# Kernel optimization log

Hardware: AMD Instinct MI355X
Metric: run time of the kernel (lower is better)

Reference implementation:

```python
import jax, jax.numpy as jnp
import numpy as np

N_MELS = 20
NUM_FRAMES = 32
FRAME_LEN = 512
SR = NUM_FRAMES * FRAME_LEN  # 16384
EPS = np.finfo(np.float64).eps  # matches np.finfo(float).eps in original


def _mel_filters(n_fft, sr, n_mels, fmin, fmax):
    """Replicates librosa.filters.mel(..., htk=False, norm=None) in pure numpy."""
    f_sp = 200.0 / 3.0
    min_log_hz = 1000.0
    min_log_mel = min_log_hz / f_sp
    logstep = np.log(6.4) / 27.0

    def hz_to_mel(f):
        f = np.asarray(f, dtype=np.float64)
        return np.where(f >= min_log_hz,
                        min_log_mel + np.log(np.maximum(f, 1e-10) / min_log_hz) / logstep,
                        f / f_sp)

    def mel_to_hz(m):
        m = np.asarray(m, dtype=np.float64)
        return np.where(m >= min_log_mel,
                        min_log_hz * np.exp(logstep * (m - min_log_mel)),
                        f_sp * m)

    fftfreqs = np.linspace(0.0, sr / 2.0, 1 + n_fft // 2)
    mels = np.linspace(hz_to_mel(fmin), hz_to_mel(fmax), n_mels + 2)
    mel_f = mel_to_hz(mels)
    fdiff = np.diff(mel_f)
    ramps = mel_f[:, None] - fftfreqs[None, :]
    lower = -ramps[:-2] / fdiff[:-1, None]
    upper = ramps[2:] / fdiff[1:, None]
    weights = np.maximum(0.0, np.minimum(lower, upper))  # norm=None -> no scaling
    return weights.astype(np.float32)  # (n_mels, 1+n_fft//2)


def setup_inputs() -> dict:
    key = jax.random.key(0)
    inputs = jax.random.normal(key, (4096, NUM_FRAMES, FRAME_LEN), dtype=jnp.float32)
    filter_banks = jnp.asarray(_mel_filters(FRAME_LEN, SR, N_MELS, 0.0, SR / 2.0 + 1.0))
    hw = jnp.asarray(np.hamming(FRAME_LEN).astype(np.float32))
    return {"inputs": inputs, "filter_banks": filter_banks, "hw": hw}


def reference(inputs, filter_banks, hw):
    # Hamming window + forward-normalized rFFT; original squares only the REAL part.
    fft_real = jnp.fft.rfft(inputs * hw, norm="forward").real  # (B, 32, 257)
    mag = fft_real * fft_real
    mels = jnp.einsum("mf,btf->btm", filter_banks, mag)  # (B, 32, 20)
    mels = jnp.where(mels == 0, jnp.float32(EPS), mels)
    log_mels = jnp.log2(mels)
    return jnp.floor(log_mels)[..., None]  # (B, 32, 20, 1)
```

## Files before the change

### kernel.cpp

```cpp
#include <hip/hip_runtime.h>
#include <math.h>


#define MARGIN_L2 1.0e-3f
#define IDX(e) ((e) + ((e) >> 3))
#define WCSTRIDE 20

__device__ __forceinline__ float4 f4add(float4 a, float4 b) {
    return make_float4(a.x + b.x, a.y + b.y, a.z + b.z, a.w + b.w);
}
__device__ __forceinline__ float4 f4sub(float4 a, float4 b) {
    return make_float4(a.x - b.x, a.y - b.y, a.z - b.z, a.w - b.w);
}
__device__ __forceinline__ float4 cmulc4(float2 w, float4 z) {
    return make_float4(w.x * z.x + w.y * z.y, w.x * z.y - w.y * z.x,
                       w.x * z.z + w.y * z.w, w.x * z.w - w.y * z.z);
}
__device__ __forceinline__ double2 d2add(double2 a, double2 b) {
    return make_double2(a.x + b.x, a.y + b.y);
}
__device__ __forceinline__ double2 d2sub(double2 a, double2 b) {
    return make_double2(a.x - b.x, a.y - b.y);
}
__device__ __forceinline__ double2 cmulcd(double2 w, double2 z) {
    return make_double2(w.x * z.x + w.y * z.y, w.x * z.y - w.y * z.x);
}

__device__ __forceinline__ void bfly4(int s, int l, float2 w1, float2 w2,
                                      float4 x1, float4 y1, float4 x2, float4 y2,
                                      float4* dst) {
    const int j = l >> s;
    const int r = l & ((1 << s) - 1);
    const float4 u1 = f4add(x1, y1);
    const float4 v1 = cmulc4(w1, f4sub(x1, y1));
    const float4 u2 = f4add(x2, y2);
    const float4 m  = cmulc4(w1, f4sub(x2, y2));
    const float4 v2 = make_float4(m.y, -m.x, m.w, -m.z);
    const float4 o0 = f4add(u1, u2);
    const float4 o1 = cmulc4(w2, f4sub(u1, u2));
    const float4 o2 = f4add(v1, v2);
    const float4 o3 = cmulc4(w2, f4sub(v1, v2));
    const int eb = (j << (s + 2)) + r;
    dst[IDX(eb)]            = o0;
    dst[IDX(eb + (1 << s))] = o2;
    dst[IDX(eb + (2 << s))] = o1;
    dst[IDX(eb + (3 << s))] = o3;
}

__device__ __forceinline__ void bfly4d(int s, int l, double2 w1, double2 w2,
                                       double2 x1, double2 y1, double2 x2,
                                       double2 y2, double2* dst) {
    const int j = l >> s;
    const int r = l & ((1 << s) - 1);
    const double2 u1 = d2add(x1, y1);
    const double2 v1 = cmulcd(w1, d2sub(x1, y1));
    const double2 u2 = d2add(x2, y2);
    const double2 m  = cmulcd(w1, d2sub(x2, y2));
    const double2 v2 = make_double2(m.y, -m.x);
    const double2 o0 = d2add(u1, u2);
    const double2 o1 = cmulcd(w2, d2sub(u1, u2));
    const double2 o2 = d2add(v1, v2);
    const double2 o3 = cmulcd(w2, d2sub(v1, v2));
    const int eb = (j << (s + 2)) + r;
    dst[IDX(eb)]            = o0;
    dst[IDX(eb + (1 << s))] = o2;
    dst[IDX(eb + (2 << s))] = o1;
    dst[IDX(eb + (3 << s))] = o3;
}

__device__ __forceinline__ void load_stage0(
    const float* __restrict__ x, int f0, int f1, int l,
    float2 h0, float2 h1, float2 h2, float2 h3,
    float2 w1, float2 w2, float4* W)
{
    const float2* xa = (const float2*)(x + (size_t)f0 * 512);
    const float2* xb = (const float2*)(x + (size_t)f1 * 512);
    const float2 a0 = xa[l],       a1 = xa[l + 64];
    const float2 a2 = xa[l + 128], a3 = xa[l + 192];
    const float2 b0 = xb[l],       b1 = xb[l + 64];
    const float2 b2 = xb[l + 128], b3 = xb[l + 192];
    const float4 x1 = make_float4(a0.x * h0.x, a0.y * h0.y,
                                  b0.x * h0.x, b0.y * h0.y);
    const float4 x2 = make_float4(a1.x * h1.x, a1.y * h1.y,
                                  b1.x * h1.x, b1.y * h1.y);
    const float4 y1 = make_float4(a2.x * h2.x, a2.y * h2.y,
                                  b2.x * h2.x, b2.y * h2.y);
    const float4 y2 = make_float4(a3.x * h3.x, a3.y * h3.y,
                                  b3.x * h3.x, b3.y * h3.y);
    bfly4(0, l, w1, w2, x1, y1, x2, y2, W);
}

__global__ void prep_full(const float* __restrict__ fb,
                          double* __restrict__ tw64,
                          float4* __restrict__ twp,
                          double4* __restrict__ twq,
                          float4* __restrict__ wc,
                          int*    __restrict__ meta,
                          unsigned* count) {
    __shared__ float2 s_tw[256];
    __shared__ double sc[256], ss[256];
    __shared__ int slo[20], shi[20], sg0[20], sng[20];
    const int t = threadIdx.x;
    double s, c;
    sincospi((double)t * (1.0 / 256.0), &s, &c);
    tw64[t]       = c;
    tw64[256 + t] = s;
    sc[t] = c; ss[t] = s;
    s_tw[t] = make_float2((float)c, (float)s);
    if (t < 20) { slo[t] = 257; shi[t] = 0; }
    __syncthreads();

    if (t < 240) {
        const int m = t / 12, part = t % 12;
        const int k0 = part * 22;
        int k1 = k0 + 22; if (k1 > 257) k1 = 257;
        int lo = 257, hi = 0;
        for (int k = k0; k < k1; k++)
            if (fb[m * 257 + k] > 0.0f) { if (k < lo) lo = k; hi = k + 1; }
        if (hi > lo) { atomicMin(&slo[m], lo); atomicMax(&shi[m], hi); }
    }
    __syncthreads();

    if (t < 20) {
        int lo = slo[t], hi = shi[t];
        if (hi <= lo) { lo = 0; hi = 1; }
        int g0 = lo >> 2;
        int ng = ((hi + 3) >> 2) - g0;
        if (ng > WCSTRIDE) ng = WCSTRIDE;
        sg0[t] = g0; sng[t] = ng;
        meta[t] = g0 | (ng << 16);
    }
    if (t < 64) {
        const float2 a0 = s_tw[2 * t],        b0 = s_tw[4 * t];
        twp[t]        = make_float4(a0.x, a0.y, b0.x, b0.y);
        const float2 a2 = s_tw[8 * (t >> 2)], b2 = s_tw[16 * (t >> 2)];
        twp[64 + t]   = make_float4(a2.x, a2.y, b2.x, b2.y);
        const float2 a4 = s_tw[32 * (t >> 4)], b4 = s_tw[64 * (t >> 4)];
        twp[128 + t]  = make_float4(a4.x, a4.y, b4.x, b4.y);
        const float2 u0 = s_tw[t],            u1 = s_tw[t + 64];
        twp[192 + t]  = make_float4(u0.x, u0.y, u1.x, u1.y);
        twq[t]       = make_double4(sc[2*t], ss[2*t], sc[4*t], ss[4*t]);
        twq[64 + t]  = make_double4(sc[8*(t>>2)],  ss[8*(t>>2)],
                                    sc[16*(t>>2)], ss[16*(t>>2)]);
        twq[128 + t] = make_double4(sc[32*(t>>4)], ss[32*(t>>4)],
                                    sc[64*(t>>4)], ss[64*(t>>4)]);
        twq[192 + t] = make_double4(sc[t], ss[t], sc[t+64], ss[t+64]);
    }
    __syncthreads();

    for (int i = t; i < 20 * WCSTRIDE; i += 256) {
        const int m = i / WCSTRIDE, j = i % WCSTRIDE;
        float4 v = make_float4(0.0f, 0.0f, 0.0f, 0.0f);
        if (j < sng[m]) {
            const int b = (sg0[m] + j) * 4;
            const float* row = fb + m * 257;
            v.x = (b + 0 < 257) ? row[b + 0] : 0.0f;
            v.y = (b + 1 < 257) ? row[b + 1] : 0.0f;
            v.z = (b + 2 < 257) ? row[b + 2] : 0.0f;
            v.w = (b + 3 < 257) ? row[b + 3] : 0.0f;
        }
        wc[i] = v;
    }
    if (count && t == 0) *count = 0;
}

__global__ void prep_tw64(double* __restrict__ tw64) {
    const int t = threadIdx.x;
    double s, c;
    sincospi((double)t * (1.0 / 256.0), &s, &c);
    tw64[t]       = c;
    tw64[256 + t] = s;
}

__global__ __launch_bounds__(256, 4) void phase1(
    const float* __restrict__ x,
    const float* __restrict__ hw,
    const float4* __restrict__ twp,
    const float4* __restrict__ wc,
    const int*    __restrict__ meta,
    float* __restrict__ out,
    unsigned* __restrict__ count,
    unsigned* __restrict__ worklist)
{
    __shared__ __align__(16) float4 buf[8][288];

    const int t = threadIdx.x;
    const int w = t >> 6;
    const int l = t & 63;
    const int base = (blockIdx.x * 4 + w) * 4;
    const int fg0 = base, fg1 = base + 1, fg2 = base + 2, fg3 = base + 3;

    const float4 tp0 = twp[l];
    const float4 tp2 = twp[64 + l];
    const float4 tp4 = twp[128 + l];
    const float4 tpU = twp[192 + l];
    const float2 w0s = make_float2(tp0.x, tp0.y), w0d = make_float2(tp0.z, tp0.w);
    const float2 w2s = make_float2(tp2.x, tp2.y), w2d = make_float2(tp2.z, tp2.w);
    const float2 w4s = make_float2(tp4.x, tp4.y), w4d = make_float2(tp4.z, tp4.w);

    float4* const WA = &buf[2 * w][0];
    float4* const WB = &buf[2 * w + 1][0];

    const float2* hp = (const float2*)hw;
    const float2 h0 = hp[l],       h1 = hp[l + 64];
    const float2 h2 = hp[l + 128], h3 = hp[l + 192];

    load_stage0(x, fg0, fg1, l, h0, h1, h2, h3, w0s, w0d, WA);
    load_stage0(x, fg2, fg3, l, h0, h1, h2, h3, w0s, w0d, WB);
    __builtin_amdgcn_wave_barrier();

    {
        const float4 ax1 = WA[IDX(l)],      ay1 = WA[IDX(l + 128)];
        const float4 ax2 = WA[IDX(l + 64)], ay2 = WA[IDX(l + 192)];
        const float4 bx1 = WB[IDX(l)],      by1 = WB[IDX(l + 128)];
        const float4 bx2 = WB[IDX(l + 64)], by2 = WB[IDX(l + 192)];
        bfly4(2, l, w2s, w2d, ax1, ay1, ax2, ay2, WA);
        bfly4(2, l, w2s, w2d, bx1, by1, bx2, by2, WB);
        __builtin_amdgcn_wave_barrier();
    }
    {
        const float4 ax1 = WA[IDX(l)],      ay1 = WA[IDX(l + 128)];
        const float4 ax2 = WA[IDX(l + 64)], ay2 = WA[IDX(l + 192)];
        const float4 bx1 = WB[IDX(l)],      by1 = WB[IDX(l + 128)];
        const float4 bx2 = WB[IDX(l + 64)], by2 = WB[IDX(l + 192)];
        bfly4(4, l, w4s, w4d, ax1, ay1, ax2, ay2, WA);
        bfly4(4, l, w4s, w4d, bx1, by1, bx2, by2, WB);
        __builtin_amdgcn_wave_barrier();
    }
    {
        const float4 ax1 = WA[IDX(l)],      ay1 = WA[IDX(l + 128)];
        const float4 ax2 = WA[IDX(l + 64)], ay2 = WA[IDX(l + 192)];
        const float4 bx1 = WB[IDX(l)],      by1 = WB[IDX(l + 128)];
        const float4 bx2 = WB[IDX(l + 64)], by2 = WB[IDX(l + 192)];
        {
            const float4 u1 = f4add(ax1, ay1);
            const float4 v1 = f4sub(ax1, ay1);
            const float4 u2 = f4add(ax2, ay2);
            const float4 m  = f4sub(ax2, ay2);
            const float4 v2 = make_float4(m.y, -m.x, m.w, -m.z);
            WA[IDX(l)]       = f4add(u1, u2);
            WA[IDX(l + 64)]  = f4add(v1, v2);
            WA[IDX(l + 128)] = f4sub(u1, u2);
            WA[IDX(l + 192)] = f4sub(v1, v2);
        }
        {
            const float4 u1 = f4add(bx1, by1);
            const float4 v1 = f4sub(bx1, by1);
            const float4 u2 = f4add(bx2, by2);
            const float4 m  = f4sub(bx2, by2);
            const float4 v2 = make_float4(m.y, -m.x, m.w, -m.z);
            WB[IDX(l)]       = f4add(u1, u2);
            WB[IDX(l + 64)]  = f4add(v1, v2);
            WB[IDX(l + 128)] = f4sub(u1, u2);
            WB[IDX(l + 192)] = f4sub(v1, v2);
        }
    }
    __builtin_amdgcn_wave_barrier();

    float2* const pwrA = (float2*)WA;
    float2* const pwrB = (float2*)WB;
    {
        const float4 zk0A = WA[IDX(l)];
        const float4 zc0A = WA[IDX((256 - l) & 255)];
        const float4 zk1A = WA[IDX(l + 64)];
        const float4 zc1A = WA[IDX(192 - l)];
        const float4 zmA  = WA[IDX(128)];
        const float4 zk0B = WB[IDX(l)];
        const float4 zc0B = WB[IDX((256 - l) & 255)];
        const float4 zk1B = WB[IDX(l + 64)];
        const float4 zc1B = WB[IDX(192 - l)];
        const float4 zmB  = WB[IDX(128)];
        const float2 u0 = make_float2(tpU.x, tpU.y);
        const float2 u1 = make_float2(tpU.z, tpU.w);
        __builtin_amdgcn_wave_barrier();

#define UNTANGLE_PAIR(zk, zc, wk, p, kk, kc)                                 \
        {                                                                    \
            const float Sr0 = zk.x + zc.x, Si0 = zk.y + zc.y;                \
            const float Dr0 = zk.x - zc.x;                                   \
            const float Sr1 = zk.z + zc.z, Si1 = zk.w + zc.w;                \
            const float Dr1 = zk.z - zc.z;                                   \
            const float E0 = 0.5f * Sr0;                                     \
            const float T0 = 0.5f * (wk.x * Si0 - wk.y * Dr0);               \
            const float E1 = 0.5f * Sr1;                                     \
            const float T1 = 0.5f * (wk.x * Si1 - wk.y * Dr1);               \
            const float a0 = (E0 + T0) * (1.0f / 512.0f);                    \
            const float a1 = (E1 + T1) * (1.0f / 512.0f);                    \
            const float b0 = (E0 - T0) * (1.0f / 512.0f);                    \
            const float b1 = (E1 - T1) * (1.0f / 512.0f);                    \
            p[kk] = make_float2(a0 * a0, a1 * a1);                           \
            p[kc] = make_float2(b0 * b0, b1 * b1);                           \
        }
        UNTANGLE_PAIR(zk0A, zc0A, u0, pwrA, l, 256 - l)
        UNTANGLE_PAIR(zk1A, zc1A, u1, pwrA, l + 64, 192 - l)
        UNTANGLE_PAIR(zk0B, zc0B, u0, pwrB, l, 256 - l)
        UNTANGLE_PAIR(zk1B, zc1B, u1, pwrB, l + 64, 192 - l)
#undef UNTANGLE_PAIR
        if (l == 0) {
            const float vA0 = zmA.x * (1.0f / 512.0f);
            const float vA1 = zmA.z * (1.0f / 512.0f);
            pwrA[128] = make_float2(vA0 * vA0, vA1 * vA1);
            const float vB0 = zmB.x * (1.0f / 512.0f);
            const float vB1 = zmB.z * (1.0f / 512.0f);
            pwrB[128] = make_float2(vB0 * vB0, vB1 * vB1);
        }
        if (l >= 57) {
            pwrA[257 + (l - 57)] = make_float2(0.0f, 0.0f);
            pwrB[257 + (l - 57)] = make_float2(0.0f, 0.0f);
        }
    }
    __builtin_amdgcn_wave_barrier();

    float aA = 0.0f, aB = 0.0f, aC = 0.0f, aD = 0.0f;
    if (l < 60) {
        const int mel = l % 20;
        const int sub = l / 20;
        const int mw  = meta[mel];
        const int g0m = mw & 0xffff;
        const int ngm = mw >> 16;
        const float4* wrow = wc + mel * WCSTRIDE;
        const float4* pwA4 = (const float4*)pwrA + 2 * g0m;
        const float4* pwB4 = (const float4*)pwrB + 2 * g0m;
        for (int j = sub; j < ngm; j += 3) {
            const float4 w4  = wrow[j];
            const float4 qa0 = pwA4[2 * j];
            const float4 qa1 = pwA4[2 * j + 1];
            const float4 qb0 = pwB4[2 * j];
            const float4 qb1 = pwB4[2 * j + 1];
            aA = fmaf(w4.w, qa1.z, fmaf(w4.z, qa1.x,
                 fmaf(w4.y, qa0.z, fmaf(w4.x, qa0.x, aA))));
            aB = fmaf(w4.w, qa1.w, fmaf(w4.z, qa1.y,
                 fmaf(w4.y, qa0.w, fmaf(w4.x, qa0.y, aB))));
            aC = fmaf(w4.w, qb1.z, fmaf(w4.z, qb1.x,
                 fmaf(w4.y, qb0.z, fmaf(w4.x, qb0.x, aC))));
            aD = fmaf(w4.w, qb1.w, fmaf(w4.z, qb1.y,
                 fmaf(w4.y, qb0.w, fmaf(w4.x, qb0.y, aD))));
        }
    }
    const float pA1 = __shfl(aA, l + 20), pA2 = __shfl(aA, l + 40);
    const float pB1 = __shfl(aB, l + 20), pB2 = __shfl(aB, l + 40);
    const float pC1 = __shfl(aC, l + 20), pC2 = __shfl(aC, l + 40);
    const float pD1 = __shfl(aD, l + 20), pD2 = __shfl(aD, l + 40);

    int fl0 = 0, fl1 = 0, fl2 = 0, fl3 = 0;
    if (l < 20) {
#define FINISH(acc, p1, p2, fg, flag)                                        \
        {                                                                    \
            const float v = acc + p1 + p2;                                   \
            float fl;                                                        \
            if (v < 1e-30f) { fl = -52.0f; flag = 1; }                       \
            else {                                                           \
                const float l2 = log2f(v);                                   \
                fl = floorf(l2);                                             \
                flag = (l2 - fl < MARGIN_L2) | ((fl + 1.0f - l2) < MARGIN_L2);\
            }                                                                \
            out[(size_t)fg * 20 + l] = fl;                                   \
        }
        FINISH(aA, pA1, pA2, fg0, fl0)
        FINISH(aB, pB1, pB2, fg1, fl1)
        FINISH(aC, pC1, pC2, fg2, fl2)
        FINISH(aD, pD1, pD2, fg3, fl3)
#undef FINISH
    }
    const unsigned long long b0 = __ballot(fl0);
    const unsigned long long b1 = __ballot(fl1);
    const unsigned long long b2 = __ballot(fl2);
    const unsigned long long b3 = __ballot(fl3);
    if (l == 0) {
        const unsigned nf = (b0 != 0ULL) + (b1 != 0ULL)
                          + (b2 != 0ULL) + (b3 != 0ULL);
        if (nf) {
            unsigned idx = atomicAdd(count, nf);
            if (b0 != 0ULL) worklist[idx++] = (unsigned)fg0;
            if (b1 != 0ULL) worklist[idx++] = (unsigned)fg1;
            if (b2 != 0ULL) worklist[idx++] = (unsigned)fg2;
            if (b3 != 0ULL) worklist[idx]   = (unsigned)fg3;
        }
    }
}

__global__ __launch_bounds__(256, 4) void phase2_wl(
    const float* __restrict__ x,
    const float* __restrict__ hw,
    const double4* __restrict__ twq,
    const float4* __restrict__ wc,
    const int*    __restrict__ meta,
    const unsigned* __restrict__ count,
    const unsigned* __restrict__ worklist,
    float* __restrict__ out)
{
    __shared__ __align__(16) double2 dbuf[4][288];

    const int t = threadIdx.x;
    const int w = t >> 6;
    const int l = t & 63;
    double2* const W = &dbuf[w][0];
    double* const pwr = (double*)W;

    const unsigned n = *count;
    const unsigned stride = gridDim.x * 4;
    for (unsigned i = blockIdx.x * 4 + (unsigned)w; i < n; i += stride) {
        const int f = (int)worklist[i];

        {
            const double4 tq = twq[l];
            const float2* xa = (const float2*)(x + (size_t)f * 512);
            const float2* hp = (const float2*)hw;
            const float2 a0 = xa[l],       a1 = xa[l + 64];
            const float2 a2 = xa[l + 128], a3 = xa[l + 192];
            const float2 h0 = hp[l],       h1 = hp[l + 64];
            const float2 h2 = hp[l + 128], h3 = hp[l + 192];
            const double2 x1 = make_double2((double)a0.x * (double)h0.x,
                                            (double)a0.y * (double)h0.y);
            const double2 x2 = make_double2((double)a1.x * (double)h1.x,
                                            (double)a1.y * (double)h1.y);
            const double2 y1 = make_double2((double)a2.x * (double)h2.x,
                                            (double)a2.y * (double)h2.y);
            const double2 y2 = make_double2((double)a3.x * (double)h3.x,
                                            (double)a3.y * (double)h3.y);
            bfly4d(0, l, make_double2(tq.x, tq.y), make_double2(tq.z, tq.w),
                   x1, y1, x2, y2, W);
        }
        __builtin_amdgcn_wave_barrier();
        {
            const double4 tq = twq[64 + l];
            const double2 x1 = W[IDX(l)],      y1 = W[IDX(l + 128)];
            const double2 x2 = W[IDX(l + 64)], y2 = W[IDX(l + 192)];
            bfly4d(2, l, make_double2(tq.x, tq.y), make_double2(tq.z, tq.w),
                   x1, y1, x2, y2, W);
        }
        __builtin_amdgcn_wave_barrier();
        {
            const double4 tq = twq[128 + l];
            const double2 x1 = W[IDX(l)],      y1 = W[IDX(l + 128)];
            const double2 x2 = W[IDX(l + 64)], y2 = W[IDX(l + 192)];
            bfly4d(4, l, make_double2(tq.x, tq.y), make_double2(tq.z, tq.w),
                   x1, y1, x2, y2, W);
        }
        __builtin_amdgcn_wave_barrier();
        {
            const double2 x1 = W[IDX(l)],      y1 = W[IDX(l + 128)];
            const double2 x2 = W[IDX(l + 64)], y2 = W[IDX(l + 192)];
            const double2 u1 = d2add(x1, y1);
            const double2 v1 = d2sub(x1, y1);
            const double2 u2 = d2add(x2, y2);
            const double2 m  = d2sub(x2, y2);
            const double2 v2 = make_double2(m.y, -m.x);
            W[IDX(l)]       = d2add(u1, u2);
            W[IDX(l + 64)]  = d2add(v1, v2);
            W[IDX(l + 128)] = d2sub(u1, u2);
            W[IDX(l + 192)] = d2sub(v1, v2);
        }
        __builtin_amdgcn_wave_barrier();
        {
            const double4 tq = twq[192 + l];
            const double2 zk0 = W[IDX(l)];
            const double2 zc0 = W[IDX((256 - l) & 255)];
            const double2 zk1 = W[IDX(l + 64)];
            const double2 zc1 = W[IDX(192 - l)];
            const double2 zm  = W[IDX(128)];
            __builtin_amdgcn_wave_barrier();
            {
                const double Sr = zk0.x + zc0.x, Si = zk0.y + zc0.y;
                const double Dr = zk0.x - zc0.x;
                const double E = 0.5 * Sr, T = 0.5 * (tq.x * Si - tq.y * Dr);
                const double a = (E + T) * (1.0 / 512.0);
                const double b = (E - T) * (1.0 / 512.0);
                pwr[l]       = a * a;
                pwr[256 - l] = b * b;
            }
            {
                const double Sr = zk1.x + zc1.x, Si = zk1.y + zc1.y;
                const double Dr = zk1.x - zc1.x;
                const double E = 0.5 * Sr, T = 0.5 * (tq.z * Si - tq.w * Dr);
                const double a = (E + T) * (1.0 / 512.0);
                const double b = (E - T) * (1.0 / 512.0);
                pwr[l + 64]  = a * a;
                pwr[192 - l] = b * b;
            }
            if (l == 0) {
                const double v = zm.x * (1.0 / 512.0);
                pwr[128] = v * v;
            }
            if (l < 3) pwr[257 + l] = 0.0;
        }
        __builtin_amdgcn_wave_barrier();

        double acc = 0.0;
        if (l < 60) {
            const int mel = l % 20;
            const int sub = l / 20;
            const int mw  = meta[mel];
            const int g0m = mw & 0xffff;
            const int ngm = mw >> 16;
            const float4* wrow = wc + mel * WCSTRIDE;
            const double2* pw2 = (const double2*)pwr + 2 * g0m;
            for (int j = sub; j < ngm; j += 3) {
                const float4 w4 = wrow[j];
                const double2 q0 = pw2[2 * j];
                const double2 q1 = pw2[2 * j + 1];
                acc = fma((double)w4.x, q0.x, acc);
                acc = fma((double)w4.y, q0.y, acc);
                acc = fma((double)w4.z, q1.x, acc);
                acc = fma((double)w4.w, q1.y, acc);
            }
        }
        const double p1 = __shfl(acc, l + 20);
        const double p2 = __shfl(acc, l + 40);
        if (l < 20) {
            double v = acc + p1 + p2;
            if (v == 0.0) v = 2.220446049250313e-16;
            out[(size_t)f * 20 + l] = (float)floor(log2(v));
        }
        __builtin_amdgcn_wave_barrier();
    }
}

__global__ __launch_bounds__(256) void f64_all(
    const float*  __restrict__ x,
    const float*  __restrict__ fb,
    const float*  __restrict__ hw,
    const double* __restrict__ tw,
    float* __restrict__ out)
{
    __shared__ double Are[256], Aim[256], Bre[256], Bim[256];
    __shared__ double ltc[256], lts[256];
    __shared__ double pwr[257];

    const int t = threadIdx.x;
    const int f = blockIdx.x;

    ltc[t] = tw[t];
    lts[t] = tw[256 + t];
    {
        const float2 xv = ((const float2*)x)[(size_t)f * 256 + t];
        const float2 hv = ((const float2*)hw)[t];
        Are[t] = (double)xv.x * (double)hv.x;
        Aim[t] = (double)xv.y * (double)hv.y;
    }
    __syncthreads();

    double* sre = Are; double* sim = Aim;
    double* dre = Bre; double* dim = Bim;
    const int p = t & 127;
    const int which = t >> 7;
#pragma unroll
    for (int s = 0; s < 8; s++) {
        const int j = p >> s;
        const double ar = sre[p],       ai = sim[p];
        const double br = sre[p + 128], bi = sim[p + 128];
        double orr, oi;
        int dpos;
        if (which) {
            const int idx = j << (s + 1);
            const double wr = ltc[idx];
            const double wi = -lts[idx];
            const double ur = ar - br, ui = ai - bi;
            orr = wr * ur - wi * ui;
            oi  = wr * ui + wi * ur;
            dpos = p + ((j + 1) << s);
        } else {
            orr = ar + br;
            oi  = ai + bi;
            dpos = p + (j << s);
        }
        dre[dpos] = orr;
        dim[dpos] = oi;
        __syncthreads();
        double* tmp;
        tmp = sre; sre = dre; dre = tmp;
        tmp = sim; sim = dim; dim = tmp;
    }

    {
        const double a = sre[t], b = sim[t];
        const int t2 = (256 - t) & 255;
        const double c = sre[t2], d = sim[t2];
        const double rex = 0.5 * (a + c)
                         + 0.5 * (ltc[t] * (b + d) - lts[t] * (a - c));
        const double v = rex * (1.0 / 512.0);
        pwr[t] = v * v;
        if (t == 0) {
            const double vn = (a - b) * (1.0 / 512.0);
            pwr[256] = vn * vn;
        }
    }
    __syncthreads();

    if (t < 160) {
        const int mel = t >> 3;
        const int sub = t & 7;
        const float* wrow = fb + mel * 257;
        double acc = 0.0;
        for (int k = sub; k < 257; k += 8)
            acc = fma((double)wrow[k], pwr[k], acc);
        acc += __shfl_down(acc, 4, 8);
        acc += __shfl_down(acc, 2, 8);
        acc += __shfl_down(acc, 1, 8);
        if (sub == 0) {
            double v = acc;
            if (v == 0.0) v = 2.220446049250313e-16;
            out[(size_t)f * 20 + mel] = (float)floor(log2(v));
        }
    }
}

extern "C" void kernel_launch(void* const* d_in, const int* in_sizes, int n_in,
                              void* d_out, int out_size, void* d_ws, size_t ws_size,
                              hipStream_t stream) {
    const float* x  = (const float*)d_in[0];
    const float* fb = (const float*)d_in[1];
    const float* hw = (const float*)d_in[2];
    float* out = (float*)d_out;

    const int frames = in_sizes[0] / 512;

    char* ws = (char*)d_ws;
    double*  tw64 = (double*)ws;
    float4*  twp  = (float4*)(ws + 4096);
    float4*  wc   = (float4*)(ws + 8192);
    int*     meta = (int*)(ws + 14592);
    double4* twq  = (double4*)(ws + 16384);

    const size_t T1 = 32832 + 4 * (size_t)frames;

    if (ws_size >= T1 && (frames % 16) == 0) {
        unsigned* count    = (unsigned*)(ws + 32768);
        unsigned* worklist = (unsigned*)(ws + 32832);
        prep_full<<<1, 256, 0, stream>>>(fb, tw64, twp, twq, wc, meta, count);
        phase1<<<frames / 16, 256, 0, stream>>>(x, hw, twp, wc, meta, out,
                                                count, worklist);
        phase2_wl<<<2048, 256, 0, stream>>>(x, hw, twq, wc, meta,
                                            count, worklist, out);
    } else {
        prep_tw64<<<1, 256, 0, stream>>>(tw64);
        f64_all<<<frames, 256, 0, stream>>>(x, fb, hw, tw64, out);
    }
}
```

Measured before the change: 378.5 us.

## Fuse f64 repair of borderline frames into phase1, drop worklist kernel

Frames whose float32 log2 result falls near an integer boundary are no longer pushed to a global worklist for a separate double-precision kernel. Each wave now recomputes its flagged frames in double precision inline, through a noinline device function that reuses the wave's shared buffer. This removes the third kernel launch, the atomic worklist append and the count reset. The cost is that flagged frames are serialized inside phase1 waves, and the extra code may raise register or occupancy pressure in phase1.

```diff
diff --git a/kernel.cpp b/kernel.cpp
--- a/kernel.cpp
+++ b/kernel.cpp
@@ -90,21 +90,138 @@
     bfly4(0, l, w1, w2, x1, y1, x2, y2, W);
 }
 
+__device__ __attribute__((noinline)) void repair_f64(
+    const float* __restrict__ x, const float* __restrict__ hw,
+    const double4* __restrict__ twq, const float4* __restrict__ wc,
+    const int* __restrict__ meta, float* __restrict__ out,
+    int f, int l, double2* W)
+{
+    double* const pwr = (double*)W;
+
+    {
+        const double4 tq = twq[l];
+        const float2* xa = (const float2*)(x + (size_t)f * 512);
+        const float2* hp = (const float2*)hw;
+        const float2 a0 = xa[l],       a1 = xa[l + 64];
+        const float2 a2 = xa[l + 128], a3 = xa[l + 192];
+        const float2 h0 = hp[l],       h1 = hp[l + 64];
+        const float2 h2 = hp[l + 128], h3 = hp[l + 192];
+        const double2 x1 = make_double2((double)a0.x * (double)h0.x,
+                                        (double)a0.y * (double)h0.y);
+        const double2 x2 = make_double2((double)a1.x * (double)h1.x,
+                                        (double)a1.y * (double)h1.y);
+        const double2 y1 = make_double2((double)a2.x * (double)h2.x,
+                                        (double)a2.y * (double)h2.y);
+        const double2 y2 = make_double2((double)a3.x * (double)h3.x,
+                                        (double)a3.y * (double)h3.y);
+        bfly4d(0, l, make_double2(tq.x, tq.y), make_double2(tq.z, tq.w),
+               x1, y1, x2, y2, W);
+    }
+    __builtin_amdgcn_wave_barrier();
+    {
+        const double4 tq = twq[64 + l];
+        const double2 x1 = W[IDX(l)],      y1 = W[IDX(l + 128)];
+        const double2 x2 = W[IDX(l + 64)], y2 = W[IDX(l + 192)];
+        bfly4d(2, l, make_double2(tq.x, tq.y), make_double2(tq.z, tq.w),
+               x1, y1, x2, y2, W);
+    }
+    __builtin_amdgcn_wave_barrier();
+    {
+        const double4 tq = twq[128 + l];
+        const double2 x1 = W[IDX(l)],      y1 = W[IDX(l + 128)];
+        const double2 x2 = W[IDX(l + 64)], y2 = W[IDX(l + 192)];
+        bfly4d(4, l, make_double2(tq.x, tq.y), make_double2(tq.z, tq.w),
+               x1, y1, x2, y2, W);
+    }
+    __builtin_amdgcn_wave_barrier();
+    {
+        const double2 x1 = W[IDX(l)],      y1 = W[IDX(l + 128)];
+        const double2 x2 = W[IDX(l + 64)], y2 = W[IDX(l + 192)];
+        const double2 u1 = d2add(x1, y1);
+        const double2 v1 = d2sub(x1, y1);
+        const double2 u2 = d2add(x2, y2);
+        const double2 m  = d2sub(x2, y2);
+        const double2 v2 = make_double2(m.y, -m.x);
+        W[IDX(l)]       = d2add(u1, u2);
+        W[IDX(l + 64)]  = d2add(v1, v2);
+        W[IDX(l + 128)] = d2sub(u1, u2);
+        W[IDX(l + 192)] = d2sub(v1, v2);
+    }
+    __builtin_amdgcn_wave_barrier();
+    {
+        const double4 tq = twq[192 + l];
+        const double2 zk0 = W[IDX(l)];
+        const double2 zc0 = W[IDX((256 - l) & 255)];
+        const double2 zk1 = W[IDX(l + 64)];
+        const double2 zc1 = W[IDX(192 - l)];
+        const double2 zm  = W[IDX(128)];
+        __builtin_amdgcn_wave_barrier();
+        {
+            const double Sr = zk0.x + zc0.x, Si = zk0.y + zc0.y;
+            const double Dr = zk0.x - zc0.x;
+            const double E = 0.5 * Sr, T = 0.5 * (tq.x * Si - tq.y * Dr);
+            const double a = (E + T) * (1.0 / 512.0);
+            const double b = (E - T) * (1.0 / 512.0);
+            pwr[l]       = a * a;
+            pwr[256 - l] = b * b;
+        }
+        {
+            const double Sr = zk1.x + zc1.x, Si = zk1.y + zc1.y;
+            const double Dr = zk1.x - zc1.x;
+            const double E = 0.5 * Sr, T = 0.5 * (tq.z * Si - tq.w * Dr);
+            const double a = (E + T) * (1.0 / 512.0);
+            const double b = (E - T) * (1.0 / 512.0);
+            pwr[l + 64]  = a * a;
+            pwr[192 - l] = b * b;
+        }
+        if (l == 0) {
+            const double v = zm.x * (1.0 / 512.0);
+            pwr[128] = v * v;
+        }
+        if (l < 3) pwr[257 + l] = 0.0;
+    }
+    __builtin_amdgcn_wave_barrier();
+
+    double acc = 0.0;
+    if (l < 60) {
+        const int mel = l % 20;
+        const int sub = l / 20;
+        const int mw  = meta[mel];
+        const int g0m = mw & 0xffff;
+        const int ngm = mw >> 16;
+        const float4* wrow = wc + mel * WCSTRIDE;
+        const double2* pw2 = (const double2*)pwr + 2 * g0m;
+        for (int j = sub; j < ngm; j += 3) {
+            const float4 w4 = wrow[j];
+            const double2 q0 = pw2[2 * j];
+            const double2 q1 = pw2[2 * j + 1];
+            acc = fma((double)w4.x, q0.x, acc);
+            acc = fma((double)w4.y, q0.y, acc);
+            acc = fma((double)w4.z, q1.x, acc);
+            acc = fma((double)w4.w, q1.y, acc);
+        }
+    }
+    const double p1 = __shfl(acc, l + 20);
+    const double p2 = __shfl(acc, l + 40);
+    if (l < 20) {
+        double v = acc + p1 + p2;
+        if (v == 0.0) v = 2.220446049250313e-16;
+        out[(size_t)f * 20 + l] = (float)floor(log2(v));
+    }
+    __builtin_amdgcn_wave_barrier();
+}
+
 __global__ void prep_full(const float* __restrict__ fb,
-                          double* __restrict__ tw64,
                           float4* __restrict__ twp,
                           double4* __restrict__ twq,
                           float4* __restrict__ wc,
-                          int*    __restrict__ meta,
-                          unsigned* count) {
+                          int*    __restrict__ meta) {
     __shared__ float2 s_tw[256];
     __shared__ double sc[256], ss[256];
     __shared__ int slo[20], shi[20], sg0[20], sng[20];
     const int t = threadIdx.x;
     double s, c;
     sincospi((double)t * (1.0 / 256.0), &s, &c);
-    tw64[t]       = c;
-    tw64[256 + t] = s;
     sc[t] = c; ss[t] = s;
     s_tw[t] = make_float2((float)c, (float)s);
     if (t < 20) { slo[t] = 257; shi[t] = 0; }
@@ -161,7 +278,6 @@
         }
         wc[i] = v;
     }
-    if (count && t == 0) *count = 0;
 }
 
 __global__ void prep_tw64(double* __restrict__ tw64) {
@@ -176,11 +292,10 @@
     const float* __restrict__ x,
     const float* __restrict__ hw,
     const float4* __restrict__ twp,
+    const double4* __restrict__ twq,
     const float4* __restrict__ wc,
     const int*    __restrict__ meta,
-    float* __restrict__ out,
-    unsigned* __restrict__ count,
-    unsigned* __restrict__ worklist)
+    float* __restrict__ out)
 {
     __shared__ __align__(16) float4 buf[8][288];
 
@@ -366,153 +481,14 @@
     const unsigned long long b1 = __ballot(fl1);
     const unsigned long long b2 = __ballot(fl2);
     const unsigned long long b3 = __ballot(fl3);
-    if (l == 0) {
-        const unsigned nf = (b0 != 0ULL) + (b1 != 0ULL)
-                          + (b2 != 0ULL) + (b3 != 0ULL);
-        if (nf) {
-            unsigned idx = atomicAdd(count, nf);
-            if (b0 != 0ULL) worklist[idx++] = (unsigned)fg0;
-            if (b1 != 0ULL) worklist[idx++] = (unsigned)fg1;
-            if (b2 != 0ULL) worklist[idx++] = (unsigned)fg2;
-            if (b3 != 0ULL) worklist[idx]   = (unsigned)fg3;
-        }
-    }
-}
-
-__global__ __launch_bounds__(256, 4) void phase2_wl(
-    const float* __restrict__ x,
-    const float* __restrict__ hw,
-    const double4* __restrict__ twq,
-    const float4* __restrict__ wc,
-    const int*    __restrict__ meta,
-    const unsigned* __restrict__ count,
-    const unsigned* __restrict__ worklist,
-    float* __restrict__ out)
-{
-    __shared__ __align__(16) double2 dbuf[4][288];
-
-    const int t = threadIdx.x;
-    const int w = t >> 6;
-    const int l = t & 63;
-    double2* const W = &dbuf[w][0];
-    double* const pwr = (double*)W;
-
-    const unsigned n = *count;
-    const unsigned stride = gridDim.x * 4;
-    for (unsigned i = blockIdx.x * 4 + (unsigned)w; i < n; i += stride) {
-        const int f = (int)worklist[i];
-
-        {
-            const double4 tq = twq[l];
-            const float2* xa = (const float2*)(x + (size_t)f * 512);
-            const float2* hp = (const float2*)hw;
-            const float2 a0 = xa[l],       a1 = xa[l + 64];
-            const float2 a2 = xa[l + 128], a3 = xa[l + 192];
-            const float2 h0 = hp[l],       h1 = hp[l + 64];
-            const float2 h2 = hp[l + 128], h3 = hp[l + 192];
-            const double2 x1 = make_double2((double)a0.x * (double)h0.x,
-                                            (double)a0.y * (double)h0.y);
-            const double2 x2 = make_double2((double)a1.x * (double)h1.x,
-                                            (double)a1.y * (double)h1.y);
-            const double2 y1 = make_double2((double)a2.x * (double)h2.x,
-                                            (double)a2.y * (double)h2.y);
-            const double2 y2 = make_double2((double)a3.x * (double)h3.x,
-                                            (double)a3.y * (double)h3.y);
-            bfly4d(0, l, make_double2(tq.x, tq.y), make_double2(tq.z, tq.w),
-                   x1, y1, x2, y2, W);
-        }
+
+    if ((b0 | b1 | b2 | b3) != 0ULL) {
         __builtin_amdgcn_wave_barrier();
-        {
-            const double4 tq = twq[64 + l];
-            const double2 x1 = W[IDX(l)],      y1 = W[IDX(l + 128)];
-            const double2 x2 = W[IDX(l + 64)], y2 = W[IDX(l + 192)];
-            bfly4d(2, l, make_double2(tq.x, tq.y), make_double2(tq.z, tq.w),
-                   x1, y1, x2, y2, W);
-        }
-        __builtin_amdgcn_wave_barrier();
-        {
-            const double4 tq = twq[128 + l];
-            const double2 x1 = W[IDX(l)],      y1 = W[IDX(l + 128)];
-            const double2 x2 = W[IDX(l + 64)], y2 = W[IDX(l + 192)];
-            bfly4d(4, l, make_double2(tq.x, tq.y), make_double2(tq.z, tq.w),
-                   x1, y1, x2, y2, W);
-        }
-        __builtin_amdgcn_wave_barrier();
-        {
-            const double2 x1 = W[IDX(l)],      y1 = W[IDX(l + 128)];
-            const double2 x2 = W[IDX(l + 64)], y2 = W[IDX(l + 192)];
-            const double2 u1 = d2add(x1, y1);
-            const double2 v1 = d2sub(x1, y1);
-            const double2 u2 = d2add(x2, y2);
-            const double2 m  = d2sub(x2, y2);
-            const double2 v2 = make_double2(m.y, -m.x);
-            W[IDX(l)]       = d2add(u1, u2);
-            W[IDX(l + 64)]  = d2add(v1, v2);
-            W[IDX(l + 128)] = d2sub(u1, u2);
-            W[IDX(l + 192)] = d2sub(v1, v2);
-        }
-        __builtin_amdgcn_wave_barrier();
-        {
-            const double4 tq = twq[192 + l];
-            const double2 zk0 = W[IDX(l)];
-            const double2 zc0 = W[IDX((256 - l) & 255)];
-            const double2 zk1 = W[IDX(l + 64)];
-            const double2 zc1 = W[IDX(192 - l)];
-            const double2 zm  = W[IDX(128)];
-            __builtin_amdgcn_wave_barrier();
-            {
-                const double Sr = zk0.x + zc0.x, Si = zk0.y + zc0.y;
-                const double Dr = zk0.x - zc0.x;
-                const double E = 0.5 * Sr, T = 0.5 * (tq.x * Si - tq.y * Dr);
-                const double a = (E + T) * (1.0 / 512.0);
-                const double b = (E - T) * (1.0 / 512.0);
-                pwr[l]       = a * a;
-                pwr[256 - l] = b * b;
-            }
-            {
-                const double Sr = zk1.x + zc1.x, Si = zk1.y + zc1.y;
-                const double Dr = zk1.x - zc1.x;
-                const double E = 0.5 * Sr, T = 0.5 * (tq.z * Si - tq.w * Dr);
-                const double a = (E + T) * (1.0 / 512.0);
-                const double b = (E - T) * (1.0 / 512.0);
-                pwr[l + 64]  = a * a;
-                pwr[192 - l] = b * b;
-            }
-            if (l == 0) {
-                const double v = zm.x * (1.0 / 512.0);
-                pwr[128] = v * v;
-            }
-            if (l < 3) pwr[257 + l] = 0.0;
-        }
-        __builtin_amdgcn_wave_barrier();
-
-        double acc = 0.0;
-        if (l < 60) {
-            const int mel = l % 20;
-            const int sub = l / 20;
-            const int mw  = meta[mel];
-            const int g0m = mw & 0xffff;
-            const int ngm = mw >> 16;
-            const float4* wrow = wc + mel * WCSTRIDE;
-            const double2* pw2 = (const double2*)pwr + 2 * g0m;
-            for (int j = sub; j < ngm; j += 3) {
-                const float4 w4 = wrow[j];
-                const double2 q0 = pw2[2 * j];
-                const double2 q1 = pw2[2 * j + 1];
-                acc = fma((double)w4.x, q0.x, acc);
-                acc = fma((double)w4.y, q0.y, acc);
-                acc = fma((double)w4.z, q1.x, acc);
-                acc = fma((double)w4.w, q1.y, acc);
-            }
-        }
-        const double p1 = __shfl(acc, l + 20);
-        const double p2 = __shfl(acc, l + 40);
-        if (l < 20) {
-            double v = acc + p1 + p2;
-            if (v == 0.0) v = 2.220446049250313e-16;
-            out[(size_t)f * 20 + l] = (float)floor(log2(v));
-        }
-        __builtin_amdgcn_wave_barrier();
+        double2* const DW = (double2*)WA;
+        if (b0 != 0ULL) repair_f64(x, hw, twq, wc, meta, out, fg0, l, DW);
+        if (b1 != 0ULL) repair_f64(x, hw, twq, wc, meta, out, fg1, l, DW);
+        if (b2 != 0ULL) repair_f64(x, hw, twq, wc, meta, out, fg2, l, DW);
+        if (b3 != 0ULL) repair_f64(x, hw, twq, wc, meta, out, fg3, l, DW);
     }
 }
 
@@ -616,22 +592,15 @@
     const int frames = in_sizes[0] / 512;
 
     char* ws = (char*)d_ws;
+    float4*  twp  = (float4*)ws;
+    double4* twq  = (double4*)(ws + 4096);
+    float4*  wc   = (float4*)(ws + 12288);
+    int*     meta = (int*)(ws + 18688);
     double*  tw64 = (double*)ws;
-    float4*  twp  = (float4*)(ws + 4096);
-    float4*  wc   = (float4*)(ws + 8192);
-    int*     meta = (int*)(ws + 14592);
-    double4* twq  = (double4*)(ws + 16384);
-
-    const size_t T1 = 32832 + 4 * (size_t)frames;
-
-    if (ws_size >= T1 && (frames % 16) == 0) {
-        unsigned* count    = (unsigned*)(ws + 32768);
-        unsigned* worklist = (unsigned*)(ws + 32832);
-        prep_full<<<1, 256, 0, stream>>>(fb, tw64, twp, twq, wc, meta, count);
-        phase1<<<frames / 16, 256, 0, stream>>>(x, hw, twp, wc, meta, out,
-                                                count, worklist);
-        phase2_wl<<<2048, 256, 0, stream>>>(x, hw, twq, wc, meta,
-                                            count, worklist, out);
+
+    if (ws_size >= 32768 && (frames % 16) == 0) {
+        prep_full<<<1, 256, 0, stream>>>(fb, twp, twq, wc, meta);
+        phase1<<<frames / 16, 256, 0, stream>>>(x, hw, twp, twq, wc, meta, out);
     } else {
         prep_tw64<<<1, 256, 0, stream>>>(tw64);
         f64_all<<<frames, 256, 0, stream>>>(x, fb, hw, tw64, out);
```

Result: no change. 377.9 us (-0.2%).
